# Performance work log

Hardware: AMD Instinct MI355X
Metric: run time of the kernel (lower is better)

## Reference

```python
import jax, jax.numpy as jnp
import numpy as np

H = 1024   # hidden_dim
L = 2      # n_layers
V = 512    # dict_size['target']
B = 256    # batch
S = 512    # encoder seq len
IN = 64    # maxlen['input'][0] = encoder input feature dim
T = 64     # maxlen['target'] = decoder steps


def setup_inputs() -> dict:
    key = jax.random.key(0)
    ks = jax.random.split(key, 16)
    def p(k, shape):
        return jax.random.normal(k, shape, jnp.float32) * 0.05
    emb = p(ks[0], (V, H)).at[0].set(0.0)  # padding_idx=0 row is zero
    return dict(
        x=jax.random.normal(ks[1], (B, S, IN), jnp.float32),
        emb=emb,
        enc_Wih0=p(ks[2], (3 * H, IN)), enc_Whh0=p(ks[3], (3 * H, H)),
        enc_bih0=p(ks[4], (3 * H,)),   enc_bhh0=p(ks[5], (3 * H,)),
        enc_Wih1=p(ks[6], (3 * H, H)), enc_Whh1=p(ks[7], (3 * H, H)),
        enc_bih1=p(ks[8], (3 * H,)),   enc_bhh1=p(ks[9], (3 * H,)),
        dec_Wih=p(ks[10], (L, 3 * H, H)), dec_Whh=p(ks[11], (L, 3 * H, H)),
        dec_bih=p(ks[12], (L, 3 * H)),    dec_bhh=p(ks[13], (L, 3 * H)),
        fc_W=p(ks[14], (V, H)), fc_b=p(ks[15], (V,)),
    )


def gru_cell(x, h, Wih, Whh, bih, bhh):
    # torch GRU cell: r,z,n gate ordering
    gx = x @ Wih.T + bih            # (B, 3H)
    gh = h @ Whh.T + bhh            # (B, 3H)
    rx, zx, nx = jnp.split(gx, 3, axis=-1)
    rh, zh, nh = jnp.split(gh, 3, axis=-1)
    r = jax.nn.sigmoid(rx + rh)
    z = jax.nn.sigmoid(zx + zh)
    n = jnp.tanh(nx + r * nh)
    return (1.0 - z) * n + z * h


def reference(x, emb, enc_Wih0, enc_Whh0, enc_bih0, enc_bhh0,
              enc_Wih1, enc_Whh1, enc_bih1, enc_bhh1,
              dec_Wih, dec_Whh, dec_bih, dec_bhh, fc_W, fc_b):
    b = x.shape[0]
    # ---------- encoder: 2-layer unidirectional GRU ----------
    seq = jnp.swapaxes(x, 0, 1)  # (S, B, IN) time-major for scan
    enc_params = [(enc_Wih0, enc_Whh0, enc_bih0, enc_bhh0),
                  (enc_Wih1, enc_Whh1, enc_bih1, enc_bhh1)]
    finals = []
    for (Wih, Whh, bih, bhh) in enc_params:
        h0 = jnp.zeros((b, H), seq.dtype)
        def step(h, xt, Wih=Wih, Whh=Whh, bih=bih, bhh=bhh):
            hn = gru_cell(xt, h, Wih, Whh, bih, bhh)
            return hn, hn
        hT, seq = jax.lax.scan(step, h0, seq)
        finals.append(hT)
    hidden = jnp.stack(finals)  # (L, B, H)

    tok0 = jnp.zeros((b,), jnp.int32)  # start token 0 (== <pad>)

    def dec_step(carry, _):
        hcur, tok = carry
        inp = emb[tok]                       # (B, H) embedding lookup
        new_h = []
        for l in range(L):
            hn = gru_cell(inp, hcur[l], dec_Wih[l], dec_Whh[l],
                          dec_bih[l], dec_bhh[l])
            new_h.append(hn)
            inp = hn
        logits = inp @ fc_W.T + fc_b         # (B, V)
        tok = jnp.argmax(logits, axis=-1).astype(jnp.int32)
        return (jnp.stack(new_h), tok), logits

    (h_fin, _), logits_seq = jax.lax.scan(dec_step, (hidden, tok0), None, length=T)
    out = jnp.swapaxes(logits_seq, 0, 1)     # (B, T, V)
    return out, h_fin
```

## Files before the change

kernel.cpp:

```cpp
#include <hip/hip_runtime.h>
#include <math.h>

namespace {

constexpr int BSZ = 256;
constexpr int SEQ = 512;
constexpr int KIN = 64;
constexpr int HID = 1024;
constexpr int GD  = 3072;
constexpr int VOC = 512;
constexpr int TT  = 64;

typedef _Float16 half_t;
typedef _Float16 half4 __attribute__((ext_vector_type(4)));
typedef _Float16 half8 __attribute__((ext_vector_type(8)));
typedef float f32x4 __attribute__((ext_vector_type(4)));

constexpr float LOSCL = 4096.f;
constexpr float LOINV = 1.f / 4096.f;

__device__ __forceinline__ void decode_mc(int bb, int& m0, int& c0) {
  int c_lo = bb & 7, rest = bb >> 3;
  int m = rest & 7, c_hi = rest >> 3;
  m0 = m * 32;
  c0 = (c_hi * 8 + c_lo) * 32;
}

__global__ __launch_bounds__(256) void swz_kernel(
    const float* __restrict__ src, half_t* __restrict__ hi,
    half_t* __restrict__ lo, int NG, int NKCH, int HIDR, int n)
{
  int i = blockIdx.x * 256 + threadIdx.x;
  if (i >= n) return;
  int j = i & 7, l = (i >> 3) & 63;
  int frag = i >> 9;
  int g = frag % NG;
  int rest = frag / NG;
  int w4 = rest & 3;
  int rest2 = rest >> 2;
  int kc = rest2 % NKCH;
  int ct = rest2 / NKCH;
  int ldw = NKCH * 64;
  int row = g * HIDR + ct * 32 + (w4 & 1) * 16 + (l & 15);
  int col = kc * 64 + (w4 >> 1) * 32 + (l >> 4) * 8 + j;
  float f = src[(size_t)row * ldw + col];
  half_t h = (half_t)f;
  hi[i] = h;
  lo[i] = (half_t)((f - (float)h) * LOSCL);
}

__global__ __launch_bounds__(256) void xsplit_kernel(
    const float* __restrict__ x, half_t* __restrict__ xhi,
    half_t* __restrict__ xlo, int n4)
{
  int i = blockIdx.x * 256 + threadIdx.x;
  if (i >= n4) return;
  float4 v = ((const float4*)x)[i];
  float vv[4] = {v.x, v.y, v.z, v.w};
  half4 h, lo;
  #pragma unroll
  for (int j = 0; j < 4; ++j) {
    float f = vv[j]; half_t hh = (half_t)f;
    h[j] = hh; lo[j] = (half_t)((f - (float)hh) * LOSCL);
  }
  ((half4*)xhi)[i] = h;
  ((half4*)xlo)[i] = lo;
}

typedef half_t AldsT[2][2][32][136];

template<int NG, int G2>
__device__ __forceinline__ void gemm_swz128(
    const half_t* __restrict__ Ahi, const half_t* __restrict__ Alo,
    size_t lda, int nch,
    const half_t* __restrict__ Whi, const half_t* __restrict__ Wlo,
    int ct, int kc0, int nkch_tot, int m0,
    f32x4 (&aH)[4][2], f32x4 (&aL)[4][2], AldsT& Alds)
{
  const int tid = threadIdx.x;
  const int wv = tid >> 6, l = tid & 63, lr = l & 15, lk = l >> 4;
  const int colg = wv & 1, ksg = wv >> 1;
  const int arow = tid >> 3, aseg = tid & 7;
  const half_t* ahp = Ahi + (size_t)(m0 + arow) * lda + aseg * 16;
  const half_t* alp = Alo + (size_t)(m0 + arow) * lda + aseg * 16;

  const size_t FR = (size_t)NG * 512;
  const size_t S2STR = 2 * FR;
  const size_t CSTR = 8 * FR;
  const size_t bbase =
      (((size_t)(ct * nkch_tot + kc0 + ksg)) * 4 + colg) * FR + l * 8;
  const half_t* bph = Whi + bbase;
  const half_t* bpl = Wlo + bbase;

  half8 paE[4], paO[4];
  half8 bhE[2 * NG], blE[2 * NG], bhO[2 * NG], blO[2 * NG];
  paE[0] = *(const half8*)(ahp);
  paE[1] = *(const half8*)(ahp + 8);
  paE[2] = *(const half8*)(alp);
  paE[3] = *(const half8*)(alp + 8);
  #pragma unroll
  for (int s2 = 0; s2 < 2; ++s2)
    #pragma unroll
    for (int g = 0; g < NG; ++g) {
      bhE[s2 * NG + g] = *(const half8*)(bph + s2 * S2STR + g * 512);
      blE[s2 * NG + g] = *(const half8*)(bpl + s2 * S2STR + g * 512);
    }

#define SWC(pac, bhc, blc, pan, bhn, bln, CH, BUF)                            \
  {                                                                           \
    *(half8*)&Alds[BUF][0][arow][aseg * 16] = pac[0];                         \
    *(half8*)&Alds[BUF][0][arow][aseg * 16 + 8] = pac[1];                     \
    *(half8*)&Alds[BUF][1][arow][aseg * 16] = pac[2];                         \
    *(half8*)&Alds[BUF][1][arow][aseg * 16 + 8] = pac[3];                     \
    __syncthreads();                                                          \
    if ((CH) + 1 < nch) {                                                     \
      const size_t aco = (size_t)((CH) + 1) * 128;                            \
      pan[0] = *(const half8*)(ahp + aco);                                    \
      pan[1] = *(const half8*)(ahp + aco + 8);                                \
      pan[2] = *(const half8*)(alp + aco);                                    \
      pan[3] = *(const half8*)(alp + aco + 8);                                \
      _Pragma("unroll") for (int s2 = 0; s2 < 2; ++s2)                        \
        _Pragma("unroll") for (int g = 0; g < NG; ++g) {                      \
          bhn[s2 * NG + g] =                                                  \
              *(const half8*)(bph + ((CH) + 1) * CSTR + s2 * S2STR + g * 512);\
          bln[s2 * NG + g] =                                                  \
              *(const half8*)(bpl + ((CH) + 1) * CSTR + s2 * S2STR + g * 512);\
        }                                                                     \
    }                                                                         \
    _Pragma("unroll") for (int s2 = 0; s2 < 2; ++s2) {                        \
      half8 ah0 = *(const half8*)&Alds[BUF][0][lr][ksg * 64 + s2 * 32 + lk * 8];      \
      half8 ah1 = *(const half8*)&Alds[BUF][0][16 + lr][ksg * 64 + s2 * 32 + lk * 8]; \
      half8 al0 = *(const half8*)&Alds[BUF][1][lr][ksg * 64 + s2 * 32 + lk * 8];      \
      half8 al1 = *(const half8*)&Alds[BUF][1][16 + lr][ksg * 64 + s2 * 32 + lk * 8]; \
      _Pragma("unroll") for (int g = 0; g < NG; ++g) {                        \
        const int slot = (g == 2) ? G2 : g;                                   \
        half8 bh = bhc[s2 * NG + g];                                          \
        half8 bl = blc[s2 * NG + g];                                          \
        aH[slot][0] = __builtin_amdgcn_mfma_f32_16x16x32_f16(ah0, bh, aH[slot][0], 0, 0, 0); \
        aH[slot][1] = __builtin_amdgcn_mfma_f32_16x16x32_f16(ah1, bh, aH[slot][1], 0, 0, 0); \
        aL[slot][0] = __builtin_amdgcn_mfma_f32_16x16x32_f16(ah0, bl, aL[slot][0], 0, 0, 0); \
        aL[slot][0] = __builtin_amdgcn_mfma_f32_16x16x32_f16(al0, bh, aL[slot][0], 0, 0, 0); \
        aL[slot][1] = __builtin_amdgcn_mfma_f32_16x16x32_f16(ah1, bl, aL[slot][1], 0, 0, 0); \
        aL[slot][1] = __builtin_amdgcn_mfma_f32_16x16x32_f16(al1, bh, aL[slot][1], 0, 0, 0); \
      }                                                                       \
    }                                                                         \
  }

  for (int ch = 0; ch < nch; ch += 2) {
    SWC(paE, bhE, blE, paO, bhO, blO, ch, 0)
    SWC(paO, bhO, blO, paE, bhE, blE, (ch + 1), 1)
  }
#undef SWC
}

template<int NG, int G2>
__device__ __forceinline__ void gemm_swz64(
    const half_t* __restrict__ Ahi, const half_t* __restrict__ Alo,
    size_t lda,
    const half_t* __restrict__ Whi, const half_t* __restrict__ Wlo,
    int ct, int nkch_tot, int m0,
    f32x4 (&aH)[4][2], f32x4 (&aL)[4][2], AldsT& Alds)
{
  const int tid = threadIdx.x;
  const int wv = tid >> 6, l = tid & 63, lr = l & 15, lk = l >> 4;
  const int colg = wv & 1, ksg = wv >> 1;
  const int arow = tid >> 3, aseg = tid & 7;
  const half_t* ahp = Ahi + (size_t)(m0 + arow) * lda + aseg * 8;
  const half_t* alp = Alo + (size_t)(m0 + arow) * lda + aseg * 8;

  const size_t FR = (size_t)NG * 512;
  const size_t bbase =
      (((size_t)(ct * nkch_tot)) * 4 + (colg + 2 * ksg)) * FR + l * 8;
  half8 bh[NG], bl[NG];
  #pragma unroll
  for (int g = 0; g < NG; ++g) {
    bh[g] = *(const half8*)(Whi + bbase + g * 512);
    bl[g] = *(const half8*)(Wlo + bbase + g * 512);
  }
  half8 hi8 = *(const half8*)(ahp);
  half8 lo8 = *(const half8*)(alp);
  *(half8*)&Alds[0][0][arow][aseg * 8] = hi8;
  *(half8*)&Alds[0][1][arow][aseg * 8] = lo8;
  __syncthreads();
  half8 ah0 = *(const half8*)&Alds[0][0][lr][ksg * 32 + lk * 8];
  half8 ah1 = *(const half8*)&Alds[0][0][16 + lr][ksg * 32 + lk * 8];
  half8 al0 = *(const half8*)&Alds[0][1][lr][ksg * 32 + lk * 8];
  half8 al1 = *(const half8*)&Alds[0][1][16 + lr][ksg * 32 + lk * 8];
  #pragma unroll
  for (int g = 0; g < NG; ++g) {
    const int slot = (g == 2) ? G2 : g;
    aH[slot][0] = __builtin_amdgcn_mfma_f32_16x16x32_f16(ah0, bh[g], aH[slot][0], 0, 0, 0);
    aH[slot][1] = __builtin_amdgcn_mfma_f32_16x16x32_f16(ah1, bh[g], aH[slot][1], 0, 0, 0);
    aL[slot][0] = __builtin_amdgcn_mfma_f32_16x16x32_f16(ah0, bl[g], aL[slot][0], 0, 0, 0);
    aL[slot][0] = __builtin_amdgcn_mfma_f32_16x16x32_f16(al0, bh[g], aL[slot][0], 0, 0, 0);
    aL[slot][1] = __builtin_amdgcn_mfma_f32_16x16x32_f16(ah1, bl[g], aL[slot][1], 0, 0, 0);
    aL[slot][1] = __builtin_amdgcn_mfma_f32_16x16x32_f16(al1, bh[g], aL[slot][1], 0, 0, 0);
  }
}

template<int NS>
__device__ __forceinline__ void combine_ks(
    f32x4 (&aH)[4][2], f32x4 (&aL)[4][2], float* __restrict__ xch)
{
  const int tid = threadIdx.x;
  const int wv = tid >> 6, l = tid & 63;
  const int colg = wv & 1, ksg = wv >> 1;
  #pragma unroll
  for (int q = 0; q < NS; ++q)
    #pragma unroll
    for (int mf = 0; mf < 2; ++mf)
      aH[q][mf] = aH[q][mf] + aL[q][mf] * LOINV;
  __syncthreads();
  float* base = xch + ((size_t)colg * 64 + l) * (NS * 8);
  if (ksg == 1) {
    #pragma unroll
    for (int q = 0; q < NS; ++q)
      #pragma unroll
      for (int mf = 0; mf < 2; ++mf)
        *(f32x4*)(base + q * 8 + mf * 4) = aH[q][mf];
  }
  __syncthreads();
  if (ksg == 0) {
    #pragma unroll
    for (int q = 0; q < NS; ++q)
      #pragma unroll
      for (int mf = 0; mf < 2; ++mf)
        aH[q][mf] = aH[q][mf] + *(const f32x4*)(base + q * 8 + mf * 4);
  }
}

__device__ __forceinline__ void gru_epi32s(
    f32x4 (&vv)[4][2],
    const float* __restrict__ bih, const float* __restrict__ bhh,
    const float* __restrict__ hprev, float* __restrict__ hout,
    half_t* __restrict__ houthi, half_t* __restrict__ houtlo,
    int m0, int c0)
{
  const int tid = threadIdx.x;
  if (tid >= 128) return;
  const int wv = tid >> 6, l = tid & 63, lr = l & 15, lk = l >> 4;
  const int c = c0 + (wv & 1) * 16 + lr;
  float bhr = bhh[c], bhz = bhh[HID + c], bhn = bhh[2 * HID + c];
  float bir = 0.f, biz = 0.f, bin = 0.f;
  if (bih) { bir = bih[c]; biz = bih[HID + c]; bin = bih[2 * HID + c]; }
  #pragma unroll
  for (int mf = 0; mf < 2; ++mf) {
    #pragma unroll
    for (int i = 0; i < 4; ++i) {
      int b = m0 + mf * 16 + lk * 4 + i;
      float rs = vv[0][mf][i] + bhr + bir;
      float zs = vv[1][mf][i] + bhz + biz;
      float nx = vv[2][mf][i] + bin;
      float nh = vv[3][mf][i] + bhn;
      float r = 1.f / (1.f + expf(-rs));
      float z = 1.f / (1.f + expf(-zs));
      float n = tanhf(nx + r * nh);
      float o = (1.f - z) * n + z * hprev[(size_t)b * HID + c];
      hout[(size_t)b * HID + c] = o;
      half_t hv = (half_t)o;
      houthi[(size_t)b * HID + c] = hv;
      houtlo[(size_t)b * HID + c] = (half_t)((o - (float)hv) * LOSCL);
    }
  }
}

__device__ __forceinline__ void write_partials32(
    f32x4 (&vv)[4][2], int s2, float* __restrict__ P, int m0, int c0)
{
  const int tid = threadIdx.x;
  if (tid >= 128) return;
  const int wv = tid >> 6, l = tid & 63, lr = l & 15, lk = l >> 4;
  const int c = c0 + (wv & 1) * 16 + lr;
  #pragma unroll
  for (int g = 0; g < 3; ++g) {
    const int slot = (g == 2) ? s2 : g;
    #pragma unroll
    for (int mf = 0; mf < 2; ++mf) {
      #pragma unroll
      for (int i = 0; i < 4; ++i) {
        int b = m0 + mf * 16 + lk * 4 + i;
        P[((size_t)g * BSZ + b) * HID + c] = vv[slot][mf][i];
      }
    }
  }
}

#define INIT_ACC(aH, aL)                                  \
  _Pragma("unroll") for (int q = 0; q < 4; ++q)           \
    _Pragma("unroll") for (int m_ = 0; m_ < 2; ++m_) {    \
      aH[q][m_] = (f32x4){0.f, 0.f, 0.f, 0.f};            \
      aL[q][m_] = (f32x4){0.f, 0.f, 0.f, 0.f};            \
    }

__global__ __launch_bounds__(256, 2) void enc_step_mfma(
    int s, const half_t* __restrict__ xhi, const half_t* __restrict__ xlo,
    const half_t* __restrict__ Wih0h, const half_t* __restrict__ Wih0l,
    const float* __restrict__ bih0,
    const half_t* __restrict__ Whh0h, const half_t* __restrict__ Whh0l,
    const float* __restrict__ bhh0,
    const half_t* __restrict__ Wih1h, const half_t* __restrict__ Wih1l,
    const float* __restrict__ bih1,
    const half_t* __restrict__ Whh1h, const half_t* __restrict__ Whh1l,
    const float* __restrict__ bhh1,
    float* __restrict__ h0f, float* __restrict__ h1f,
    half_t* __restrict__ h0hi, half_t* __restrict__ h0lo,
    half_t* __restrict__ h1hi, half_t* __restrict__ h1lo)
{
  __shared__ __align__(16) AldsT Alds;
  f32x4 aH[4][2], aL[4][2];
  INIT_ACC(aH, aL)
  const size_t BH = (size_t)BSZ * HID;
  int blk = blockIdx.x;
  if (blk < 256) {
    if (s >= SEQ) return;
    int m0, c0; decode_mc(blk, m0, c0);
    int ct = c0 >> 5;
    const size_t sp = ((s + 1) & 1) * BH, so = (s & 1) * BH;
    gemm_swz128<3, 3>(h0hi + sp, h0lo + sp, HID, 8, Whh0h, Whh0l,
                      ct, 0, 16, m0, aH, aL, Alds);
    gemm_swz64<3, 2>(xhi + (size_t)s * KIN, xlo + (size_t)s * KIN,
                     (size_t)SEQ * KIN, Wih0h, Wih0l, ct, 1, m0, aH, aL, Alds);
    combine_ks<4>(aH, aL, (float*)Alds);
    gru_epi32s(aH, bih0, bhh0, h0f + sp, h0f + so, h0hi + so, h0lo + so,
               m0, c0);
  } else {
    if (s < 1) return;
    int u = s - 1;
    int m0, c0; decode_mc(blk - 256, m0, c0);
    int ct = c0 >> 5;
    const size_t up = ((u + 1) & 1) * BH, uo = (u & 1) * BH;
    gemm_swz128<3, 3>(h1hi + up, h1lo + up, HID, 8, Whh1h, Whh1l,
                      ct, 0, 16, m0, aH, aL, Alds);
    gemm_swz128<3, 2>(h0hi + uo, h0lo + uo, HID, 8, Wih1h, Wih1l,
                      ct, 0, 16, m0, aH, aL, Alds);
    combine_ks<4>(aH, aL, (float*)Alds);
    gru_epi32s(aH, bih1, bhh1, h1f + up, h1f + uo, h1hi + uo, h1lo + uo,
               m0, c0);
  }
}

__global__ __launch_bounds__(256, 2) void gru0_main(
    const half_t* __restrict__ hphi, const half_t* __restrict__ hplo,
    const half_t* __restrict__ Whhh, const half_t* __restrict__ Whhl,
    float* __restrict__ Pg)
{
  __shared__ __align__(16) AldsT Alds;
  f32x4 aH[4][2], aL[4][2];
  INIT_ACC(aH, aL)
  int bb = blockIdx.x;
  int kh = bb >> 8;
  int m0, c0; decode_mc(bb & 255, m0, c0);
  int ct = c0 >> 5;
  gemm_swz128<3, 3>(hphi + kh * 512, hplo + kh * 512, HID, 4, Whhh, Whhl,
                    ct, kh * 8, 16, m0, aH, aL, Alds);
  combine_ks<4>(aH, aL, (float*)Alds);
  write_partials32(aH, 3, Pg + (size_t)kh * 3 * BSZ * HID, m0, c0);
}

__global__ __launch_bounds__(256) void gru0_epi(
    const float* __restrict__ Pg, const float* __restrict__ bhh,
    const float* __restrict__ E, const int* __restrict__ tok,
    const float* __restrict__ hprev, float* __restrict__ hout,
    half_t* __restrict__ houthi, half_t* __restrict__ houtlo)
{
  int idx = (blockIdx.x * 256 + threadIdx.x) * 4;
  int b = idx >> 10, c = idx & 1023;
  const size_t BH3 = (size_t)3 * BSZ * HID;
  float4 r0 = *(const float4*)&Pg[((size_t)0 * BSZ + b) * HID + c];
  float4 z0 = *(const float4*)&Pg[((size_t)1 * BSZ + b) * HID + c];
  float4 n0 = *(const float4*)&Pg[((size_t)2 * BSZ + b) * HID + c];
  float4 r1 = *(const float4*)&Pg[BH3 + ((size_t)0 * BSZ + b) * HID + c];
  float4 z1 = *(const float4*)&Pg[BH3 + ((size_t)1 * BSZ + b) * HID + c];
  float4 n1 = *(const float4*)&Pg[BH3 + ((size_t)2 * BSZ + b) * HID + c];
  const float* Er = E + (size_t)tok[b] * GD;
  float4 exr = *(const float4*)&Er[c];
  float4 exz = *(const float4*)&Er[HID + c];
  float4 exn = *(const float4*)&Er[2 * HID + c];
  float4 hp = *(const float4*)&hprev[(size_t)b * HID + c];
  float r0v[4] = {r0.x, r0.y, r0.z, r0.w}, z0v[4] = {z0.x, z0.y, z0.z, z0.w};
  float n0v[4] = {n0.x, n0.y, n0.z, n0.w}, r1v[4] = {r1.x, r1.y, r1.z, r1.w};
  float z1v[4] = {z1.x, z1.y, z1.z, z1.w}, n1v[4] = {n1.x, n1.y, n1.z, n1.w};
  float exrv[4] = {exr.x, exr.y, exr.z, exr.w};
  float exzv[4] = {exz.x, exz.y, exz.z, exz.w};
  float exnv[4] = {exn.x, exn.y, exn.z, exn.w};
  float hpv[4] = {hp.x, hp.y, hp.z, hp.w};
  float ov[4];
  half4 hh, hl;
  #pragma unroll
  for (int j = 0; j < 4; ++j) {
    int cc = c + j;
    float rs = r0v[j] + r1v[j] + bhh[cc] + exrv[j];
    float zs = z0v[j] + z1v[j] + bhh[HID + cc] + exzv[j];
    float nh = n0v[j] + n1v[j] + bhh[2 * HID + cc];
    float r = 1.f / (1.f + expf(-rs));
    float z = 1.f / (1.f + expf(-zs));
    float n = tanhf(exnv[j] + r * nh);
    ov[j] = (1.f - z) * n + z * hpv[j];
    half_t hv = (half_t)ov[j];
    hh[j] = hv;
    hl[j] = (half_t)((ov[j] - (float)hv) * LOSCL);
  }
  float4 o; o.x = ov[0]; o.y = ov[1]; o.z = ov[2]; o.w = ov[3];
  *(float4*)&hout[(size_t)b * HID + c] = o;
  *(half4*)&houthi[(size_t)b * HID + c] = hh;
  *(half4*)&houtlo[(size_t)b * HID + c] = hl;
}

__global__ __launch_bounds__(256, 2) void dec_l1_main(
    const half_t* __restrict__ hd1hi, const half_t* __restrict__ hd1lo,
    const half_t* __restrict__ ho0hi, const half_t* __restrict__ ho0lo,
    const half_t* __restrict__ Whhh, const half_t* __restrict__ Whhl,
    const half_t* __restrict__ Wihh, const half_t* __restrict__ Wihl,
    float* __restrict__ Phh, float* __restrict__ Pih)
{
  __shared__ __align__(16) AldsT Alds;
  f32x4 aH[4][2], aL[4][2];
  INIT_ACC(aH, aL)
  int bb = blockIdx.x;
  if (bb < 256) {
    int m0, c0; decode_mc(bb, m0, c0);
    gemm_swz128<3, 3>(hd1hi, hd1lo, HID, 8, Whhh, Whhl, c0 >> 5, 0, 16, m0,
                      aH, aL, Alds);
    combine_ks<4>(aH, aL, (float*)Alds);
    write_partials32(aH, 3, Phh, m0, c0);
  } else {
    int m0, c0; decode_mc(bb - 256, m0, c0);
    gemm_swz128<3, 2>(ho0hi, ho0lo, HID, 8, Wihh, Wihl, c0 >> 5, 0, 16, m0,
                      aH, aL, Alds);
    combine_ks<4>(aH, aL, (float*)Alds);
    write_partials32(aH, 2, Pih, m0, c0);
  }
}

__global__ __launch_bounds__(256) void dec_l1_epi(
    const float* __restrict__ Phh, const float* __restrict__ Pih,
    const float* __restrict__ bih, const float* __restrict__ bhh,
    const float* __restrict__ hprev, float* __restrict__ hout,
    half_t* __restrict__ houthi, half_t* __restrict__ houtlo)
{
  int idx = (blockIdx.x * 256 + threadIdx.x) * 4;
  int b = idx >> 10, c = idx & 1023;
  float4 rh = *(const float4*)&Phh[((size_t)0 * BSZ + b) * HID + c];
  float4 zh = *(const float4*)&Phh[((size_t)1 * BSZ + b) * HID + c];
  float4 nh = *(const float4*)&Phh[((size_t)2 * BSZ + b) * HID + c];
  float4 rx = *(const float4*)&Pih[((size_t)0 * BSZ + b) * HID + c];
  float4 zx = *(const float4*)&Pih[((size_t)1 * BSZ + b) * HID + c];
  float4 nx = *(const float4*)&Pih[((size_t)2 * BSZ + b) * HID + c];
  float4 hp = *(const float4*)&hprev[(size_t)b * HID + c];
  float rhv[4] = {rh.x, rh.y, rh.z, rh.w}, zhv[4] = {zh.x, zh.y, zh.z, zh.w};
  float nhv[4] = {nh.x, nh.y, nh.z, nh.w}, rxv[4] = {rx.x, rx.y, rx.z, rx.w};
  float zxv[4] = {zx.x, zx.y, zx.z, zx.w}, nxv[4] = {nx.x, nx.y, nx.z, nx.w};
  float hpv[4] = {hp.x, hp.y, hp.z, hp.w};
  float ov[4];
  half4 hh, hl;
  #pragma unroll
  for (int j = 0; j < 4; ++j) {
    int cc = c + j;
    float r = 1.f / (1.f + expf(-(rhv[j] + rxv[j] + bhh[cc] + bih[cc])));
    float z = 1.f / (1.f + expf(-(zhv[j] + zxv[j] + bhh[HID + cc] + bih[HID + cc])));
    float n = tanhf(nxv[j] + bih[2 * HID + cc] + r * (nhv[j] + bhh[2 * HID + cc]));
    ov[j] = (1.f - z) * n + z * hpv[j];
    half_t hv = (half_t)ov[j];
    hh[j] = hv;
    hl[j] = (half_t)((ov[j] - (float)hv) * LOSCL);
  }
  float4 o; o.x = ov[0]; o.y = ov[1]; o.z = ov[2]; o.w = ov[3];
  *(float4*)&hout[(size_t)b * HID + c] = o;
  *(half4*)&houthi[(size_t)b * HID + c] = hh;
  *(half4*)&houtlo[(size_t)b * HID + c] = hl;
}

__global__ __launch_bounds__(256, 2) void fc_main(
    const half_t* __restrict__ hhi, const half_t* __restrict__ hlo,
    const half_t* __restrict__ Wh, const half_t* __restrict__ Wl,
    float* __restrict__ Pfc)
{
  __shared__ __align__(16) AldsT Alds;
  f32x4 aH[4][2], aL[4][2];
  INIT_ACC(aH, aL)
  int bb = blockIdx.x;
  int kh = bb >> 7, sub = bb & 127;
  int v_lo = sub & 7, rest = sub >> 3;
  int m = rest & 7, v_hi = rest >> 3;
  int m0 = m * 32, v0 = (v_hi * 8 + v_lo) * 32;
  gemm_swz128<1, 0>(hhi + kh * 512, hlo + kh * 512, HID, 4, Wh, Wl,
                    v0 >> 5, kh * 8, 16, m0, aH, aL, Alds);
  combine_ks<1>(aH, aL, (float*)Alds);

  const int tid = threadIdx.x;
  if (tid >= 128) return;
  const int wv = tid >> 6, l = tid & 63, lr = l & 15, lk = l >> 4;
  int v = v0 + (wv & 1) * 16 + lr;
  float* P = Pfc + (size_t)kh * BSZ * VOC;
  #pragma unroll
  for (int mf = 0; mf < 2; ++mf) {
    #pragma unroll
    for (int i = 0; i < 4; ++i) {
      int b = m0 + mf * 16 + lk * 4 + i;
      P[(size_t)b * VOC + v] = aH[0][mf][i];
    }
  }
}

__global__ __launch_bounds__(256) void fc_epi(
    const float* __restrict__ Pfc, const float* __restrict__ fcb,
    float* __restrict__ out, int t, int* __restrict__ tok)
{
  __shared__ float sv[4];
  __shared__ int si[4];
  int b = blockIdx.x, tid = threadIdx.x;
  int va = tid, vb = tid + 256;
  float lga = Pfc[(size_t)b * VOC + va] + Pfc[((size_t)BSZ + b) * VOC + va] + fcb[va];
  float lgb = Pfc[(size_t)b * VOC + vb] + Pfc[((size_t)BSZ + b) * VOC + vb] + fcb[vb];
  out[((size_t)b * TT + t) * VOC + va] = lga;
  out[((size_t)b * TT + t) * VOC + vb] = lgb;
  float best = lga; int bi = va;
  if (lgb > best) { best = lgb; bi = vb; }
  #pragma unroll
  for (int off = 1; off < 64; off <<= 1) {
    float ov = __shfl_xor(best, off);
    int oi = __shfl_xor(bi, off);
    if (ov > best || (ov == best && oi < bi)) { best = ov; bi = oi; }
  }
  int wv = tid >> 6;
  if ((tid & 63) == 0) { sv[wv] = best; si[wv] = bi; }
  __syncthreads();
  if (tid == 0) {
    #pragma unroll
    for (int w = 1; w < 4; ++w)
      if (sv[w] > best || (sv[w] == best && si[w] < bi)) { best = sv[w]; bi = si[w]; }
    tok[b] = bi;
  }
}

__global__ __launch_bounds__(256) void e0_kernel(
    const float* __restrict__ emb, const float* __restrict__ Wih,
    const float* __restrict__ bih, float* __restrict__ E0)
{
  __shared__ float As[32][34];
  __shared__ float Bs[32][68];
  int m0 = (blockIdx.x & 15) << 5;
  int c0 = (blockIdx.x >> 4) << 6;
  int tid = threadIdx.x, tx = tid & 15, ty = tid >> 4;
  float acc[2][4] = {};
  for (int k0 = 0; k0 < HID; k0 += 32) {
    { int m = tid >> 3, kq = (tid & 7) << 2;
      float4 v = *(const float4*)(emb + (size_t)(m0 + m) * HID + k0 + kq);
      As[kq+0][m] = v.x; As[kq+1][m] = v.y; As[kq+2][m] = v.z; As[kq+3][m] = v.w; }
    #pragma unroll
    for (int r = 0; r < 2; ++r) {
      int idx = (r << 8) + tid;
      int n = idx >> 3, kq = (idx & 7) << 2;
      float4 v = *(const float4*)(Wih + (size_t)(c0 + n) * HID + k0 + kq);
      Bs[kq+0][n] = v.x; Bs[kq+1][n] = v.y; Bs[kq+2][n] = v.z; Bs[kq+3][n] = v.w;
    }
    __syncthreads();
    #pragma unroll 4
    for (int k = 0; k < 32; ++k) {
      float a0 = As[k][(ty << 1)], a1 = As[k][(ty << 1) + 1];
      float4 b = *(const float4*)&Bs[k][tx << 2];
      float bb[4] = {b.x, b.y, b.z, b.w};
      #pragma unroll
      for (int j = 0; j < 4; ++j) {
        acc[0][j] = fmaf(a0, bb[j], acc[0][j]);
        acc[1][j] = fmaf(a1, bb[j], acc[1][j]);
      }
    }
    __syncthreads();
  }
  #pragma unroll
  for (int i = 0; i < 2; ++i) {
    int v = m0 + (ty << 1) + i;
    #pragma unroll
    for (int j = 0; j < 4; ++j) {
      int g = c0 + (tx << 2) + j;
      E0[(size_t)v * GD + g] = acc[i][j] + bih[g];
    }
  }
}

}

extern "C" void kernel_launch(void* const* d_in, const int* in_sizes, int n_in,
                              void* d_out, int out_size, void* d_ws, size_t ws_size,
                              hipStream_t stream)
{
  const float* x     = (const float*)d_in[0];
  const float* emb   = (const float*)d_in[1];
  const float* eWih0 = (const float*)d_in[2];
  const float* eWhh0 = (const float*)d_in[3];
  const float* ebih0 = (const float*)d_in[4];
  const float* ebhh0 = (const float*)d_in[5];
  const float* eWih1 = (const float*)d_in[6];
  const float* eWhh1 = (const float*)d_in[7];
  const float* ebih1 = (const float*)d_in[8];
  const float* ebhh1 = (const float*)d_in[9];
  const float* dWih  = (const float*)d_in[10];
  const float* dWhh  = (const float*)d_in[11];
  const float* dbih  = (const float*)d_in[12];
  const float* dbhh  = (const float*)d_in[13];
  const float* fcW   = (const float*)d_in[14];
  const float* fcb   = (const float*)d_in[15];
  float* out = (float*)d_out;

  const size_t BH = (size_t)BSZ * HID;
  const size_t XN = (size_t)BSZ * SEQ * KIN;

  char* p = (char*)d_ws;
  auto alloc = [&](size_t bytes) {
    char* r = p; p += (bytes + 255) & ~(size_t)255; return r;
  };
  float* E0   = (float*)alloc((size_t)VOC * GD * 4);
  float* h0f  = (float*)alloc(2 * BH * 4);
  float* h1f  = (float*)alloc(2 * BH * 4);
  float* hd0f = (float*)alloc(2 * BH * 4);
  float* hd1f = (float*)alloc(2 * BH * 4);
  float* Phh  = (float*)alloc(3 * BH * 4);
  float* Pih  = (float*)alloc(3 * BH * 4);
  float* Pg   = (float*)alloc(6 * BH * 4);
  float* Pfc  = (float*)alloc((size_t)2 * BSZ * VOC * 4);
  const int NW_IH0 = GD * KIN, NW = GD * HID, NW_FC = VOC * HID;
  half_t* eWih0h = (half_t*)alloc((size_t)NW_IH0 * 2);
  half_t* eWih0l = (half_t*)alloc((size_t)NW_IH0 * 2);
  half_t* eWhh0h = (half_t*)alloc((size_t)NW * 2);
  half_t* eWhh0l = (half_t*)alloc((size_t)NW * 2);
  half_t* eWih1h = (half_t*)alloc((size_t)NW * 2);
  half_t* eWih1l = (half_t*)alloc((size_t)NW * 2);
  half_t* eWhh1h = (half_t*)alloc((size_t)NW * 2);
  half_t* eWhh1l = (half_t*)alloc((size_t)NW * 2);
  half_t* dWhh0h = (half_t*)alloc((size_t)NW * 2);
  half_t* dWhh0l = (half_t*)alloc((size_t)NW * 2);
  half_t* dWhh1h = (half_t*)alloc((size_t)NW * 2);
  half_t* dWhh1l = (half_t*)alloc((size_t)NW * 2);
  half_t* dWih1h = (half_t*)alloc((size_t)NW * 2);
  half_t* dWih1l = (half_t*)alloc((size_t)NW * 2);
  half_t* fcWh   = (half_t*)alloc((size_t)NW_FC * 2);
  half_t* fcWl   = (half_t*)alloc((size_t)NW_FC * 2);
  half_t* xhi  = (half_t*)alloc(XN * 2);
  half_t* xlo  = (half_t*)alloc(XN * 2);
  half_t* h0hi = (half_t*)alloc(2 * BH * 2);
  half_t* h0lo = (half_t*)alloc(2 * BH * 2);
  half_t* h1hi = (half_t*)alloc(2 * BH * 2);
  half_t* h1lo = (half_t*)alloc(2 * BH * 2);
  half_t* d0hi = (half_t*)alloc(2 * BH * 2);
  half_t* d0lo = (half_t*)alloc(2 * BH * 2);
  half_t* d1hi = (half_t*)alloc(2 * BH * 2);
  half_t* d1lo = (half_t*)alloc(2 * BH * 2);
  int* tok = (int*)alloc(BSZ * 4);

  hipMemsetAsync(h0f + BH, 0, BH * 4, stream);
  hipMemsetAsync(h1f + BH, 0, BH * 4, stream);
  hipMemsetAsync(h0hi + BH, 0, BH * 2, stream);
  hipMemsetAsync(h0lo + BH, 0, BH * 2, stream);
  hipMemsetAsync(h1hi + BH, 0, BH * 2, stream);
  hipMemsetAsync(h1lo + BH, 0, BH * 2, stream);
  hipMemsetAsync(tok, 0, BSZ * 4, stream);

  swz_kernel<<<NW_IH0 / 256, 256, 0, stream>>>(eWih0, eWih0h, eWih0l,
                                               3, 1, HID, NW_IH0);
  swz_kernel<<<NW / 256, 256, 0, stream>>>(eWhh0, eWhh0h, eWhh0l,
                                           3, 16, HID, NW);
  swz_kernel<<<NW / 256, 256, 0, stream>>>(eWih1, eWih1h, eWih1l,
                                           3, 16, HID, NW);
  swz_kernel<<<NW / 256, 256, 0, stream>>>(eWhh1, eWhh1h, eWhh1l,
                                           3, 16, HID, NW);
  swz_kernel<<<NW / 256, 256, 0, stream>>>(dWhh, dWhh0h, dWhh0l,
                                           3, 16, HID, NW);
  swz_kernel<<<NW / 256, 256, 0, stream>>>(dWhh + (size_t)NW, dWhh1h, dWhh1l,
                                           3, 16, HID, NW);
  swz_kernel<<<NW / 256, 256, 0, stream>>>(dWih + (size_t)NW, dWih1h, dWih1l,
                                           3, 16, HID, NW);
  swz_kernel<<<NW_FC / 256, 256, 0, stream>>>(fcW, fcWh, fcWl,
                                              1, 16, VOC, NW_FC);
  xsplit_kernel<<<(int)(XN / 4 / 256), 256, 0, stream>>>(x, xhi, xlo,
                                                         (int)(XN / 4));

  e0_kernel<<<768, 256, 0, stream>>>(emb, dWih, dbih, E0);

  for (int s = 0; s <= SEQ; ++s) {
    enc_step_mfma<<<512, 256, 0, stream>>>(
        s, xhi, xlo,
        eWih0h, eWih0l, ebih0, eWhh0h, eWhh0l, ebhh0,
        eWih1h, eWih1l, ebih1, eWhh1h, eWhh1l, ebhh1,
        h0f, h1f, h0hi, h0lo, h1hi, h1lo);
  }

  hipMemcpyAsync(hd0f + BH, h0f + BH, BH * 4, hipMemcpyDeviceToDevice, stream);
  hipMemcpyAsync(hd1f + BH, h1f + BH, BH * 4, hipMemcpyDeviceToDevice, stream);
  hipMemcpyAsync(d0hi + BH, h0hi + BH, BH * 2, hipMemcpyDeviceToDevice, stream);
  hipMemcpyAsync(d0lo + BH, h0lo + BH, BH * 2, hipMemcpyDeviceToDevice, stream);
  hipMemcpyAsync(d1hi + BH, h1hi + BH, BH * 2, hipMemcpyDeviceToDevice, stream);
  hipMemcpyAsync(d1lo + BH, h1lo + BH, BH * 2, hipMemcpyDeviceToDevice, stream);

  for (int t = 0; t < TT; ++t) {
    const size_t sp = ((t + 1) & 1) * BH, so = (t & 1) * BH;
    gru0_main<<<512, 256, 0, stream>>>(d0hi + sp, d0lo + sp,
                                       dWhh0h, dWhh0l, Pg);
    gru0_epi<<<256, 256, 0, stream>>>(Pg, dbhh, E0, tok, hd0f + sp,
                                      hd0f + so, d0hi + so, d0lo + so);

    dec_l1_main<<<512, 256, 0, stream>>>(d1hi + sp, d1lo + sp,
                                         d0hi + so, d0lo + so,
                                         dWhh1h, dWhh1l, dWih1h, dWih1l,
                                         Phh, Pih);
    dec_l1_epi<<<256, 256, 0, stream>>>(Phh, Pih, dbih + GD, dbhh + GD,
                                        hd1f + sp, hd1f + so,
                                        d1hi + so, d1lo + so);
    fc_main<<<256, 256, 0, stream>>>(d1hi + so, d1lo + so, fcWh, fcWl, Pfc);
    fc_epi<<<256, 256, 0, stream>>>(Pfc, fcb, out, t, tok);
  }

  hipMemcpyAsync(out + (size_t)BSZ * TT * VOC, hd0f + BH, BH * 4,
                 hipMemcpyDeviceToDevice, stream);
  hipMemcpyAsync(out + (size_t)BSZ * TT * VOC + BH, hd1f + BH, BH * 4,
                 hipMemcpyDeviceToDevice, stream);
}
```

Baseline: 15.47 ms.

## Pipeline encoder layer-1 input projection one step ahead and split FC K four ways

The encoder schedule gains a stage. Layer-1's input-hidden GEMM on h0 is now computed one step early: it is split in K across both block halves and written as partials. Layer-1's recurrent GEMM and epilogue then run a step later and read those partials. This balances work between the layer-0 and layer-1 blocks at the cost of one extra launch and additional partial-buffer traffic. Separately, the FC GEMM is split four ways in K with 512 blocks instead of 256, and the epilogue sums four partials, which should raise parallelism in the decoder FC.

```diff
diff --git a/kernel.cpp b/kernel.cpp
--- a/kernel.cpp
+++ b/kernel.cpp
@@ -264,6 +264,46 @@
   }
 }
 
+__device__ __forceinline__ void gru_epi32p(
+    f32x4 (&vv)[4][2],
+    const float* __restrict__ Pa, const float* __restrict__ Pb,
+    const float* __restrict__ bih, const float* __restrict__ bhh,
+    const float* __restrict__ hprev, float* __restrict__ hout,
+    half_t* __restrict__ houthi, half_t* __restrict__ houtlo,
+    int m0, int c0)
+{
+  const int tid = threadIdx.x;
+  if (tid >= 128) return;
+  const int wv = tid >> 6, l = tid & 63, lr = l & 15, lk = l >> 4;
+  const int c = c0 + (wv & 1) * 16 + lr;
+  const size_t BH = (size_t)BSZ * HID;
+  float bhr = bhh[c], bhz = bhh[HID + c], bhn = bhh[2 * HID + c];
+  float bir = bih[c], biz = bih[HID + c], bin = bih[2 * HID + c];
+  #pragma unroll
+  for (int mf = 0; mf < 2; ++mf) {
+    #pragma unroll
+    for (int i = 0; i < 4; ++i) {
+      int b = m0 + mf * 16 + lk * 4 + i;
+      size_t o0 = (size_t)b * HID + c;
+      float ihr = Pa[o0] + Pb[o0];
+      float ihz = Pa[BH + o0] + Pb[BH + o0];
+      float ihn = Pa[2 * BH + o0] + Pb[2 * BH + o0];
+      float rs = vv[0][mf][i] + ihr + bhr + bir;
+      float zs = vv[1][mf][i] + ihz + bhz + biz;
+      float nx = ihn + bin;
+      float nh = vv[3][mf][i] + bhn;
+      float r = 1.f / (1.f + expf(-rs));
+      float z = 1.f / (1.f + expf(-zs));
+      float n = tanhf(nx + r * nh);
+      float o = (1.f - z) * n + z * hprev[o0];
+      hout[o0] = o;
+      half_t hv = (half_t)o;
+      houthi[o0] = hv;
+      houtlo[o0] = (half_t)((o - (float)hv) * LOSCL);
+    }
+  }
+}
+
 __device__ __forceinline__ void write_partials32(
     f32x4 (&vv)[4][2], int s2, float* __restrict__ P, int m0, int c0)
 {
@@ -304,38 +344,60 @@
     const float* __restrict__ bhh1,
     float* __restrict__ h0f, float* __restrict__ h1f,
     half_t* __restrict__ h0hi, half_t* __restrict__ h0lo,
-    half_t* __restrict__ h1hi, half_t* __restrict__ h1lo)
+    half_t* __restrict__ h1hi, half_t* __restrict__ h1lo,
+    float* __restrict__ ihPa, float* __restrict__ ihPb)
 {
   __shared__ __align__(16) AldsT Alds;
   f32x4 aH[4][2], aL[4][2];
   INIT_ACC(aH, aL)
   const size_t BH = (size_t)BSZ * HID;
+  const size_t P3 = 3 * BH;
   int blk = blockIdx.x;
   if (blk < 256) {
-    if (s >= SEQ) return;
     int m0, c0; decode_mc(blk, m0, c0);
     int ct = c0 >> 5;
-    const size_t sp = ((s + 1) & 1) * BH, so = (s & 1) * BH;
-    gemm_swz128<3, 3>(h0hi + sp, h0lo + sp, HID, 8, Whh0h, Whh0l,
-                      ct, 0, 16, m0, aH, aL, Alds);
-    gemm_swz64<3, 2>(xhi + (size_t)s * KIN, xlo + (size_t)s * KIN,
-                     (size_t)SEQ * KIN, Wih0h, Wih0l, ct, 1, m0, aH, aL, Alds);
-    combine_ks<4>(aH, aL, (float*)Alds);
-    gru_epi32s(aH, bih0, bhh0, h0f + sp, h0f + so, h0hi + so, h0lo + so,
-               m0, c0);
+    if (s < SEQ) {
+      const size_t sp = ((s + 1) & 1) * BH, so = (s & 1) * BH;
+      gemm_swz128<3, 3>(h0hi + sp, h0lo + sp, HID, 8, Whh0h, Whh0l,
+                        ct, 0, 16, m0, aH, aL, Alds);
+      gemm_swz64<3, 2>(xhi + (size_t)s * KIN, xlo + (size_t)s * KIN,
+                       (size_t)SEQ * KIN, Wih0h, Wih0l, ct, 1, m0, aH, aL,
+                       Alds);
+      combine_ks<4>(aH, aL, (float*)Alds);
+      gru_epi32s(aH, bih0, bhh0, h0f + sp, h0f + so, h0hi + so, h0lo + so,
+                 m0, c0);
+    }
+    if (s >= 1 && s <= SEQ) {
+      __syncthreads();
+      INIT_ACC(aH, aL)
+      const size_t uo = ((s - 1) & 1) * BH;
+      gemm_swz128<3, 3>(h0hi + uo, h0lo + uo, HID, 4, Wih1h, Wih1l,
+                        ct, 0, 16, m0, aH, aL, Alds);
+      combine_ks<4>(aH, aL, (float*)Alds);
+      write_partials32(aH, 3, ihPa + (size_t)((s - 1) & 1) * P3, m0, c0);
+    }
   } else {
-    if (s < 1) return;
-    int u = s - 1;
     int m0, c0; decode_mc(blk - 256, m0, c0);
     int ct = c0 >> 5;
-    const size_t up = ((u + 1) & 1) * BH, uo = (u & 1) * BH;
-    gemm_swz128<3, 3>(h1hi + up, h1lo + up, HID, 8, Whh1h, Whh1l,
-                      ct, 0, 16, m0, aH, aL, Alds);
-    gemm_swz128<3, 2>(h0hi + uo, h0lo + uo, HID, 8, Wih1h, Wih1l,
-                      ct, 0, 16, m0, aH, aL, Alds);
-    combine_ks<4>(aH, aL, (float*)Alds);
-    gru_epi32s(aH, bih1, bhh1, h1f + up, h1f + uo, h1hi + uo, h1lo + uo,
-               m0, c0);
+    if (s >= 1 && s <= SEQ) {
+      const size_t uo = ((s - 1) & 1) * BH;
+      gemm_swz128<3, 3>(h0hi + uo + 512, h0lo + uo + 512, HID, 4,
+                        Wih1h, Wih1l, ct, 8, 16, m0, aH, aL, Alds);
+      combine_ks<4>(aH, aL, (float*)Alds);
+      write_partials32(aH, 3, ihPb + (size_t)((s - 1) & 1) * P3, m0, c0);
+    }
+    if (s >= 2) {
+      __syncthreads();
+      INIT_ACC(aH, aL)
+      const size_t up = ((s - 1) & 1) * BH;
+      const size_t uo = (s & 1) * BH;
+      gemm_swz128<3, 3>(h1hi + up, h1lo + up, HID, 8, Whh1h, Whh1l,
+                        ct, 0, 16, m0, aH, aL, Alds);
+      combine_ks<4>(aH, aL, (float*)Alds);
+      gru_epi32p(aH, ihPa + (size_t)(s & 1) * P3, ihPb + (size_t)(s & 1) * P3,
+                 bih1, bhh1, h1f + up, h1f + uo, h1hi + uo, h1lo + uo,
+                 m0, c0);
+    }
   }
 }
 
@@ -483,8 +545,8 @@
   int v_lo = sub & 7, rest = sub >> 3;
   int m = rest & 7, v_hi = rest >> 3;
   int m0 = m * 32, v0 = (v_hi * 8 + v_lo) * 32;
-  gemm_swz128<1, 0>(hhi + kh * 512, hlo + kh * 512, HID, 4, Wh, Wl,
-                    v0 >> 5, kh * 8, 16, m0, aH, aL, Alds);
+  gemm_swz128<1, 0>(hhi + kh * 256, hlo + kh * 256, HID, 2, Wh, Wl,
+                    v0 >> 5, kh * 4, 16, m0, aH, aL, Alds);
   combine_ks<1>(aH, aL, (float*)Alds);
 
   const int tid = threadIdx.x;
@@ -509,9 +571,14 @@
   __shared__ float sv[4];
   __shared__ int si[4];
   int b = blockIdx.x, tid = threadIdx.x;
+  const size_t PS = (size_t)BSZ * VOC;
   int va = tid, vb = tid + 256;
-  float lga = Pfc[(size_t)b * VOC + va] + Pfc[((size_t)BSZ + b) * VOC + va] + fcb[va];
-  float lgb = Pfc[(size_t)b * VOC + vb] + Pfc[((size_t)BSZ + b) * VOC + vb] + fcb[vb];
+  float lga = fcb[va], lgb = fcb[vb];
+  #pragma unroll
+  for (int kh = 0; kh < 4; ++kh) {
+    lga += Pfc[kh * PS + (size_t)b * VOC + va];
+    lgb += Pfc[kh * PS + (size_t)b * VOC + vb];
+  }
   out[((size_t)b * TT + t) * VOC + va] = lga;
   out[((size_t)b * TT + t) * VOC + vb] = lgb;
   float best = lga; int bi = va;
@@ -618,7 +685,9 @@
   float* Phh  = (float*)alloc(3 * BH * 4);
   float* Pih  = (float*)alloc(3 * BH * 4);
   float* Pg   = (float*)alloc(6 * BH * 4);
-  float* Pfc  = (float*)alloc((size_t)2 * BSZ * VOC * 4);
+  float* Pfc  = (float*)alloc((size_t)4 * BSZ * VOC * 4);
+  float* ihPa = (float*)alloc(2 * 3 * BH * 4);
+  float* ihPb = (float*)alloc(2 * 3 * BH * 4);
   const int NW_IH0 = GD * KIN, NW = GD * HID, NW_FC = VOC * HID;
   half_t* eWih0h = (half_t*)alloc((size_t)NW_IH0 * 2);
   half_t* eWih0l = (half_t*)alloc((size_t)NW_IH0 * 2);
@@ -677,12 +746,12 @@
 
   e0_kernel<<<768, 256, 0, stream>>>(emb, dWih, dbih, E0);
 
-  for (int s = 0; s <= SEQ; ++s) {
+  for (int s = 0; s <= SEQ + 1; ++s) {
     enc_step_mfma<<<512, 256, 0, stream>>>(
         s, xhi, xlo,
         eWih0h, eWih0l, ebih0, eWhh0h, eWhh0l, ebhh0,
         eWih1h, eWih1l, ebih1, eWhh1h, eWhh1l, ebhh1,
-        h0f, h1f, h0hi, h0lo, h1hi, h1lo);
+        h0f, h1f, h0hi, h0lo, h1hi, h1lo, ihPa, ihPb);
   }
 
   hipMemcpyAsync(hd0f + BH, h0f + BH, BH * 4, hipMemcpyDeviceToDevice, stream);
@@ -706,7 +775,7 @@
     dec_l1_epi<<<256, 256, 0, stream>>>(Phh, Pih, dbih + GD, dbhh + GD,
                                         hd1f + sp, hd1f + so,
                                         d1hi + so, d1lo + so);
-    fc_main<<<256, 256, 0, stream>>>(d1hi + so, d1lo + so, fcWh, fcWl, Pfc);
+    fc_main<<<512, 256, 0, stream>>>(d1hi + so, d1lo + so, fcWh, fcWl, Pfc);
     fc_epi<<<256, 256, 0, stream>>>(Pfc, fcb, out, t, tok);
   }
 
```

After: 16.04 ms. +3.7%, slower.
